# Optimization experiments

Measured on AMD Instinct MI355X. Metric: run time of the kernel, lower is better.

The kernel has to match this reference:

```python
import jax, jax.numpy as jnp
import numpy as np

T, B, H1 = 256, 8, 512
U, H2 = 64, 512
V = 128


def setup_inputs() -> dict:
    key = jax.random.key(0)
    k1, k2, k3, k4, k5, k6 = jax.random.split(key, 6)
    f = jax.random.normal(k1, (T, B, H1), dtype=jnp.float32)
    g = jax.random.normal(k2, (B, U, H2), dtype=jnp.float32)
    f_lens = jax.random.randint(k3, (B,), 1, T + 1)
    g_lens = jax.random.randint(k4, (B,), 1, U + 1)
    W = jax.random.normal(k5, (H1 + H2, V), dtype=jnp.float32) * (1.0 / np.sqrt(H1 + H2))
    b = jax.random.normal(k6, (V,), dtype=jnp.float32) * 0.01
    return {"f": f, "f_lens": f_lens, "g": g, "g_lens": g_lens, "W": W, "b": b}


def reference(f, f_lens, g, g_lens, W, b):
    # Original: f [T,B,H1] -> [B,T,1,H1] expand, g [B,U,H2] -> [B,1,U,H2] expand,
    # concat on last dim -> [B,T,U,H1+H2], then Linear over last dim.
    # Linear(concat) == f @ W[:H1] + g @ W[H1:] + b, broadcast-summed -- same math,
    # without materializing the [B,T,U,H1+H2] intermediate.
    Wf, Wg = W[:H1], W[H1:]
    pf = jnp.einsum('tbh,hv->btv', f, Wf)          # [B,T,V]
    pg = jnp.einsum('buh,hv->buv', g, Wg)          # [B,U,V]
    h = pf[:, :, None, :] + pg[:, None, :, :] + b  # [B,T,U,V]
    return h, f_lens
```

## Files before the change

### kernel.cpp

```cpp
#include <hip/hip_runtime.h>
#include <hip/hip_bf16.h>


typedef float  f32x4 __attribute__((ext_vector_type(4)));
typedef short  bh8   __attribute__((ext_vector_type(8)));

__device__ __forceinline__ unsigned short f2bf(float x) {
    unsigned u = __float_as_uint(x);
    return (unsigned short)((u + 0x7FFFu + ((u >> 16) & 1u)) >> 16);
}

__global__ __launch_bounds__(256) void proj3(const float* __restrict__ F,
                                             const float* __restrict__ G,
                                             const float* __restrict__ W,
                                             float* __restrict__ P) {
    __shared__ float sred[4][8][128];

    const int tid = threadIdx.x;
    const int rows8 = blockIdx.x * 8;
    const bool isF = rows8 < 2048;
    const int koff = isF ? 0 : 512;
    const int w = tid >> 6, lane = tid & 63, l15 = lane & 15, cc = lane >> 4;

    const int rr = rows8 + (l15 & 7);
    const float* arow = isF ? F + (((rr & 255) << 3) + (rr >> 8)) * 512
                            : G + (rr - 2048) * 512;

    f32x4 acc[8] = {};
#pragma unroll
    for (int kk = 0; kk < 4; ++kk) {
        const int k0 = w * 128 + kk * 32 + cc * 8;
        f32x4 a0 = *reinterpret_cast<const f32x4*>(arow + k0);
        f32x4 a1 = *reinterpret_cast<const f32x4*>(arow + k0 + 4);
        bh8 av;
        av[0] = (short)f2bf(a0[0]); av[1] = (short)f2bf(a0[1]);
        av[2] = (short)f2bf(a0[2]); av[3] = (short)f2bf(a0[3]);
        av[4] = (short)f2bf(a1[0]); av[5] = (short)f2bf(a1[1]);
        av[6] = (short)f2bf(a1[2]); av[7] = (short)f2bf(a1[3]);
#pragma unroll
        for (int j = 0; j < 8; ++j) {
            const float* wsrc = W + (koff + k0) * 128 + (j * 16 + l15);
            bh8 bv;
#pragma unroll
            for (int i = 0; i < 8; ++i) bv[i] = (short)f2bf(wsrc[i * 128]);
            acc[j] = __builtin_amdgcn_mfma_f32_16x16x32_bf16(av, bv, acc[j], 0, 0, 0);
        }
    }
    if (cc < 2) {
#pragma unroll
        for (int j = 0; j < 8; ++j)
#pragma unroll
            for (int q = 0; q < 4; ++q)
                sred[w][cc * 4 + q][j * 16 + l15] = acc[j][q];
    }
    __syncthreads();

    const int row = tid >> 5, colq = tid & 31;
    f32x4 s = *reinterpret_cast<const f32x4*>(&sred[0][row][colq * 4]);
    s += *reinterpret_cast<const f32x4*>(&sred[1][row][colq * 4]);
    s += *reinterpret_cast<const f32x4*>(&sred[2][row][colq * 4]);
    s += *reinterpret_cast<const f32x4*>(&sred[3][row][colq * 4]);
    *reinterpret_cast<f32x4*>(P + (rows8 + row) * 128 + colq * 4) = s;
}

__global__ __launch_bounds__(256) void bcast(const float* __restrict__ P,
                                             const float* __restrict__ bias,
                                             const int* __restrict__ f_lens,
                                             float* __restrict__ out,
                                             int lens_off) {
    const int r   = blockIdx.x;
    const int tid = threadIdx.x;
    const int b   = r >> 8;
    const int vq  = tid & 31;
    const int u0  = tid >> 5;

    f32x4 pf = *reinterpret_cast<const f32x4*>(P + r * 128 + vq * 4);
    f32x4 bi = *reinterpret_cast<const f32x4*>(bias + vq * 4);
    pf += bi;

    const float* pg = P + (2048 + b * 64) * 128;
    float* ob = out + (size_t)r * 8192;

#pragma unroll
    for (int i = 0; i < 8; ++i) {
        int u = u0 * 8 + i;
        f32x4 v = *reinterpret_cast<const f32x4*>(pg + u * 128 + vq * 4);
        v += pf;
        *reinterpret_cast<f32x4*>(ob + u * 128 + vq * 4) = v;
    }

    if (r == 0 && tid < 8) out[lens_off + tid] = (float)f_lens[tid];
}

extern "C" void kernel_launch(void* const* d_in, const int* in_sizes, int n_in,
                              void* d_out, int out_size, void* d_ws, size_t ws_size,
                              hipStream_t stream) {
    const float* f      = (const float*)d_in[0];
    const int*   f_lens = (const int*)  d_in[1];
    const float* g      = (const float*)d_in[2];
    const float* W      = (const float*)d_in[4];
    const float* bias   = (const float*)d_in[5];
    float* out = (float*)d_out;

    float* P = (float*)d_ws;

    proj3<<<dim3(320),  dim3(256), 0, stream>>>(f, g, W, P);
    bcast<<<dim3(2048), dim3(256), 0, stream>>>(P, bias, f_lens, out, out_size - 8);
}
```

Before: 26.36 us.

## Fuse projection GEMMs and broadcast-add into one kernel with LDS-staged weights

Replaces the two-kernel pipeline (projection into a workspace, then broadcast) with a single kernel. Each block covers one batch and 8 time steps. It recomputes the g projection for its batch, computes its 8 f rows, stages bf16-converted W tiles in double-buffered LDS, then writes the broadcast sum straight to the output. This drops one launch and the workspace round-trip. In exchange, the g projection (64x512x128) is computed redundantly in every one of the 32 blocks per batch, and all of W is re-read and re-converted per block.

```diff
diff --git a/kernel.cpp b/kernel.cpp
--- a/kernel.cpp
+++ b/kernel.cpp
@@ -2,6 +2,7 @@
 #include <hip/hip_bf16.h>
 
 
+typedef float  f32x2 __attribute__((ext_vector_type(2)));
 typedef float  f32x4 __attribute__((ext_vector_type(4)));
 typedef short  bh8   __attribute__((ext_vector_type(8)));
 
@@ -10,86 +11,128 @@
     return (unsigned short)((u + 0x7FFFu + ((u >> 16) & 1u)) >> 16);
 }
 
-__global__ __launch_bounds__(256) void proj3(const float* __restrict__ F,
+__device__ __forceinline__ bh8 cvt8(f32x4 a, f32x4 b) {
+    bh8 r;
+    r[0] = (short)f2bf(a[0]); r[1] = (short)f2bf(a[1]);
+    r[2] = (short)f2bf(a[2]); r[3] = (short)f2bf(a[3]);
+    r[4] = (short)f2bf(b[0]); r[5] = (short)f2bf(b[1]);
+    r[6] = (short)f2bf(b[2]); r[7] = (short)f2bf(b[3]);
+    return r;
+}
+
+__global__ __launch_bounds__(256) void joint(const float* __restrict__ F,
                                              const float* __restrict__ G,
                                              const float* __restrict__ W,
-                                             float* __restrict__ P) {
-    __shared__ float sred[4][8][128];
-
-    const int tid = threadIdx.x;
-    const int rows8 = blockIdx.x * 8;
-    const bool isF = rows8 < 2048;
-    const int koff = isF ? 0 : 512;
-    const int w = tid >> 6, lane = tid & 63, l15 = lane & 15, cc = lane >> 4;
-
-    const int rr = rows8 + (l15 & 7);
-    const float* arow = isF ? F + (((rr & 255) << 3) + (rr >> 8)) * 512
-                            : G + (rr - 2048) * 512;
-
-    f32x4 acc[8] = {};
-#pragma unroll
-    for (int kk = 0; kk < 4; ++kk) {
-        const int k0 = w * 128 + kk * 32 + cc * 8;
-        f32x4 a0 = *reinterpret_cast<const f32x4*>(arow + k0);
-        f32x4 a1 = *reinterpret_cast<const f32x4*>(arow + k0 + 4);
-        bh8 av;
-        av[0] = (short)f2bf(a0[0]); av[1] = (short)f2bf(a0[1]);
-        av[2] = (short)f2bf(a0[2]); av[3] = (short)f2bf(a0[3]);
-        av[4] = (short)f2bf(a1[0]); av[5] = (short)f2bf(a1[1]);
-        av[6] = (short)f2bf(a1[2]); av[7] = (short)f2bf(a1[3]);
-#pragma unroll
-        for (int j = 0; j < 8; ++j) {
-            const float* wsrc = W + (koff + k0) * 128 + (j * 16 + l15);
-            bh8 bv;
-#pragma unroll
-            for (int i = 0; i < 8; ++i) bv[i] = (short)f2bf(wsrc[i * 128]);
-            acc[j] = __builtin_amdgcn_mfma_f32_16x16x32_bf16(av, bv, acc[j], 0, 0, 0);
-        }
-    }
-    if (cc < 2) {
-#pragma unroll
-        for (int j = 0; j < 8; ++j)
-#pragma unroll
-            for (int q = 0; q < 4; ++q)
-                sred[w][cc * 4 + q][j * 16 + l15] = acc[j][q];
-    }
-    __syncthreads();
-
-    const int row = tid >> 5, colq = tid & 31;
-    f32x4 s = *reinterpret_cast<const f32x4*>(&sred[0][row][colq * 4]);
-    s += *reinterpret_cast<const f32x4*>(&sred[1][row][colq * 4]);
-    s += *reinterpret_cast<const f32x4*>(&sred[2][row][colq * 4]);
-    s += *reinterpret_cast<const f32x4*>(&sred[3][row][colq * 4]);
-    *reinterpret_cast<f32x4*>(P + (rows8 + row) * 128 + colq * 4) = s;
-}
-
-__global__ __launch_bounds__(256) void bcast(const float* __restrict__ P,
                                              const float* __restrict__ bias,
                                              const int* __restrict__ f_lens,
                                              float* __restrict__ out,
                                              int lens_off) {
-    const int r   = blockIdx.x;
+    __shared__ short Bf[2][4][128][8];
+    __shared__ short Bg[2][4][128][8];
+    __shared__ float pgs[64][128];
+    __shared__ float pfs[8][128];
+
     const int tid = threadIdx.x;
-    const int b   = r >> 8;
-    const int vq  = tid & 31;
-    const int u0  = tid >> 5;
+    const int b  = blockIdx.x >> 5;
+    const int t0 = (blockIdx.x & 31) * 8;
+    const int w = tid >> 6, lane = tid & 63, l15 = lane & 15, cg = lane >> 4;
 
-    f32x4 pf = *reinterpret_cast<const f32x4*>(P + r * 128 + vq * 4);
-    f32x4 bi = *reinterpret_cast<const f32x4*>(bias + vq * 4);
-    pf += bi;
+    const int v0 = (tid & 63) * 2;
+    const float* grow = G + (b * 64 + w * 16 + l15) * 512;
+    const float* frow = F + ((t0 + (l15 & 7)) * 8 + b) * 512;
 
-    const float* pg = P + (2048 + b * 64) * 128;
-    float* ob = out + (size_t)r * 8192;
+    f32x4 accg[8] = {};
+    f32x4 accf[2] = {};
+
+    {
+        const int krow = w * 8;
+        short tf[2][8], tg[2][8];
+#pragma unroll
+        for (int r = 0; r < 8; ++r) {
+            f32x2 xf = *reinterpret_cast<const f32x2*>(W + (krow + r) * 128 + v0);
+            f32x2 xg = *reinterpret_cast<const f32x2*>(W + (512 + krow + r) * 128 + v0);
+            tf[0][r] = (short)f2bf(xf[0]); tf[1][r] = (short)f2bf(xf[1]);
+            tg[0][r] = (short)f2bf(xg[0]); tg[1][r] = (short)f2bf(xg[1]);
+        }
+#pragma unroll
+        for (int i = 0; i < 2; ++i) {
+            *reinterpret_cast<bh8*>(&Bf[0][w][v0 + i][0]) = *reinterpret_cast<bh8*>(&tf[i][0]);
+            *reinterpret_cast<bh8*>(&Bg[0][w][v0 + i][0]) = *reinterpret_cast<bh8*>(&tg[i][0]);
+        }
+    }
+    __syncthreads();
+
+    for (int s = 0; s < 16; ++s) {
+        const int d = s & 1;
+        if (s < 15) {
+            const int krow = (s + 1) * 32 + w * 8;
+            short tf[2][8], tg[2][8];
+#pragma unroll
+            for (int r = 0; r < 8; ++r) {
+                f32x2 xf = *reinterpret_cast<const f32x2*>(W + (krow + r) * 128 + v0);
+                f32x2 xg = *reinterpret_cast<const f32x2*>(W + (512 + krow + r) * 128 + v0);
+                tf[0][r] = (short)f2bf(xf[0]); tf[1][r] = (short)f2bf(xf[1]);
+                tg[0][r] = (short)f2bf(xg[0]); tg[1][r] = (short)f2bf(xg[1]);
+            }
+#pragma unroll
+            for (int i = 0; i < 2; ++i) {
+                *reinterpret_cast<bh8*>(&Bf[d ^ 1][w][v0 + i][0]) = *reinterpret_cast<bh8*>(&tf[i][0]);
+                *reinterpret_cast<bh8*>(&Bg[d ^ 1][w][v0 + i][0]) = *reinterpret_cast<bh8*>(&tg[i][0]);
+            }
+        }
+
+        const int k0 = s * 32 + cg * 8;
+        f32x4 g0 = *reinterpret_cast<const f32x4*>(grow + k0);
+        f32x4 g1 = *reinterpret_cast<const f32x4*>(grow + k0 + 4);
+        bh8 ag = cvt8(g0, g1);
+#pragma unroll
+        for (int j = 0; j < 8; ++j) {
+            bh8 bb = *reinterpret_cast<const bh8*>(&Bg[d][cg][j * 16 + l15][0]);
+            accg[j] = __builtin_amdgcn_mfma_f32_16x16x32_bf16(ag, bb, accg[j], 0, 0, 0);
+        }
+        f32x4 f0 = *reinterpret_cast<const f32x4*>(frow + k0);
+        f32x4 f1 = *reinterpret_cast<const f32x4*>(frow + k0 + 4);
+        bh8 af = cvt8(f0, f1);
+#pragma unroll
+        for (int jj = 0; jj < 2; ++jj) {
+            bh8 bb = *reinterpret_cast<const bh8*>(&Bf[d][cg][(2 * w + jj) * 16 + l15][0]);
+            accf[jj] = __builtin_amdgcn_mfma_f32_16x16x32_bf16(af, bb, accf[jj], 0, 0, 0);
+        }
+        __syncthreads();
+    }
 
 #pragma unroll
-    for (int i = 0; i < 8; ++i) {
-        int u = u0 * 8 + i;
-        f32x4 v = *reinterpret_cast<const f32x4*>(pg + u * 128 + vq * 4);
-        v += pf;
-        *reinterpret_cast<f32x4*>(ob + u * 128 + vq * 4) = v;
+    for (int j = 0; j < 8; ++j)
+#pragma unroll
+        for (int q = 0; q < 4; ++q)
+            pgs[w * 16 + cg * 4 + q][j * 16 + l15] = accg[j][q];
+    if (cg < 2) {
+#pragma unroll
+        for (int jj = 0; jj < 2; ++jj)
+#pragma unroll
+            for (int q = 0; q < 4; ++q)
+                pfs[cg * 4 + q][(2 * w + jj) * 16 + l15] = accf[jj][q];
+    }
+    __syncthreads();
+
+    const int vq = tid & 31, ug = tid >> 5;
+    const f32x4 bi = *reinterpret_cast<const f32x4*>(bias + vq * 4);
+    f32x4 pfv[8];
+#pragma unroll
+    for (int t2 = 0; t2 < 8; ++t2)
+        pfv[t2] = *reinterpret_cast<const f32x4*>(&pfs[t2][vq * 4]) + bi;
+
+    float* ob = out + (size_t)(b * 256 + t0) * 8192;
+#pragma unroll
+    for (int ui = 0; ui < 8; ++ui) {
+        const int u = ui * 8 + ug;
+        f32x4 pgv = *reinterpret_cast<const f32x4*>(&pgs[u][vq * 4]);
+#pragma unroll
+        for (int t2 = 0; t2 < 8; ++t2)
+            *reinterpret_cast<f32x4*>(ob + (t2 * 64 + u) * 128 + vq * 4) = pfv[t2] + pgv;
     }
 
-    if (r == 0 && tid < 8) out[lens_off + tid] = (float)f_lens[tid];
+    if (blockIdx.x == 0 && tid < 8) out[lens_off + tid] = (float)f_lens[tid];
 }
 
 extern "C" void kernel_launch(void* const* d_in, const int* in_sizes, int n_in,
@@ -102,8 +145,5 @@
     const float* bias   = (const float*)d_in[5];
     float* out = (float*)d_out;
 
-    float* P = (float*)d_ws;
-
-    proj3<<<dim3(320),  dim3(256), 0, stream>>>(f, g, W, P);
-    bcast<<<dim3(2048), dim3(256), 0, stream>>>(P, bias, f_lens, out, out_size - 8);
+    joint<<<dim3(256), dim3(256), 0, stream>>>(f, g, W, bias, f_lens, out, out_size - 8);
 }
```

Result: slower. 40.91 us (+55.2%).
